# Optimization experiments

Hardware: AMD Instinct MI355X
Metric: run time of the kernel (lower is better)

## Reference

```python
import jax, jax.numpy as jnp
import numpy as np

B, T, F, H = 2048, 512, 32, 16  # batch, seq, input_size, hidden_size


def _gru_layer(x, W_ih, W_hh, b_ih, b_hh):
    # x: [B, T, in]; W_ih: [3H, in]; W_hh: [3H, H]
    xg = jnp.einsum('bti,gi->btg', x, W_ih) + b_ih  # [B, T, 3H] precomputed input gates

    def step(h, xg_t):
        hg = h @ W_hh.T + b_hh                      # [B, 3H]
        xr, xz, xn = jnp.split(xg_t, 3, axis=-1)
        hr, hz, hn = jnpp_split(hg) if False else jnp.split(hg, 3, axis=-1)
        r = jax.nn.sigmoid(xr + hr)
        z = jax.nn.sigmoid(xz + hz)
        n = jnp.tanh(xn + r * hn)
        h_new = (1.0 - z) * n + z * h
        return h_new, h_new

    h0 = jnp.zeros((x.shape[0], W_hh.shape[1]), x.dtype)
    _, hs = jax.lax.scan(step, h0, jnp.swapaxes(xg, 0, 1))  # [T, B, H]
    return jnp.swapaxes(hs, 0, 1)                            # [B, T, H]


def setup_inputs() -> dict:
    key = jax.random.key(0)
    ks = jax.random.split(key, 12)
    s = 1.0 / np.sqrt(H)
    u = lambda k, shape: jax.random.uniform(k, shape, jnp.float32, -s, s)
    return {
        'x': jax.random.normal(ks[0], (B, T, F), jnp.float32),
        'W_ih0': u(ks[1], (3 * H, F)),
        'W_hh0': u(ks[2], (3 * H, H)),
        'b_ih0': u(ks[3], (3 * H,)),
        'b_hh0': u(ks[4], (3 * H,)),
        'W_ih1': u(ks[5], (3 * H, H)),
        'W_hh1': u(ks[6], (3 * H, H)),
        'b_ih1': u(ks[7], (3 * H,)),
        'b_hh1': u(ks[8], (3 * H,)),
        'fc_w': u(ks[9], (1, H)),
        'fc_b': u(ks[10], (1,)),
    }


def reference(x, W_ih0, W_hh0, b_ih0, b_hh0, W_ih1, W_hh1, b_ih1, b_hh1, fc_w, fc_b):
    h1 = _gru_layer(x, W_ih0, W_hh0, b_ih0, b_hh0)   # [B, T, H]
    h2 = _gru_layer(h1, W_ih1, W_hh1, b_ih1, b_hh1)  # [B, T, H]
    return h2[:, -1, :] @ fc_w.T + fc_b              # [B, 1]
```

## Files before the change

### kernel.cpp

```cpp
#include <hip/hip_runtime.h>

static constexpr int T_LEN = 512;

typedef _Float16 h2 __attribute__((ext_vector_type(2)));

__device__ __forceinline__ float fsigm(float x) {
    return __builtin_amdgcn_rcpf(1.0f + __expf(-x));
}
__device__ __forceinline__ float ftanh(float x) {
    return 1.0f - 2.0f * __builtin_amdgcn_rcpf(1.0f + __expf(2.0f * x));
}
template <int CTRL>
__device__ __forceinline__ float rotf(float v) {
    return __builtin_bit_cast(float,
        __builtin_amdgcn_mov_dpp(__builtin_bit_cast(int, v), CTRL, 0xf, 0xf, true));
}
template <int CTRL>
__device__ __forceinline__ unsigned rotu(unsigned v) {
    return (unsigned)__builtin_amdgcn_mov_dpp((int)v, CTRL, 0xf, 0xf, true);
}
__device__ __forceinline__ unsigned pk2(float a, float b) {
    return __builtin_bit_cast(unsigned, __builtin_amdgcn_cvt_pkrtz(a, b));
}
__device__ __forceinline__ float dot2(float acc, unsigned w, unsigned p) {
    asm("v_dot2_f32_f16 %0, %1, %2, %0" : "+v"(acc) : "v"(w), "v"(p));
    return acc;
}

__global__ __launch_bounds__(256, 1) void gru2_dot(
    const float* __restrict__ x,
    const float* __restrict__ Wih0, const float* __restrict__ Whh0,
    const float* __restrict__ bih0, const float* __restrict__ bhh0,
    const float* __restrict__ Wih1, const float* __restrict__ Whh1,
    const float* __restrict__ bih1, const float* __restrict__ bhh1,
    const float* __restrict__ fcw,  const float* __restrict__ fcb,
    float* __restrict__ out)
{
    const int tid  = threadIdx.x;
    const int w    = tid >> 6;
    const int lane = tid & 63;
    const int j    = lane & 15;
    const int bb   = (w & 1) * 4 + (lane >> 4);
    const int b    = blockIdx.x * 8 + bb;
    const bool isL0 = (w < 2);

    __shared__ float h0buf[8][8][16];

    const int d1 = (((int)rotf<0x121>((float)j)) - j) & 15;

    unsigned WX[3][16];
    unsigned WH[3][8];
    unsigned WI[3][8];
    float B_r, B_z, B_in, B_hn;

    if (isL0) {
#pragma unroll
        for (int g = 0; g < 3; ++g) {
            const int row = g * 16 + j;
#pragma unroll
            for (int m = 0; m < 16; ++m) {
                const int c = (j + m * d1) & 15;
                WX[g][m] = pk2(Wih0[row * 32 + c], Wih0[row * 32 + 16 + c]);
            }
#pragma unroll
            for (int m = 0; m < 8; ++m) {
                const int c = (j + m * d1) & 15;
                const int c8 = (c + 8) & 15;
                WH[g][m] = pk2(Whh0[row * 16 + c], Whh0[row * 16 + c8]);
            }
        }
        B_r  = bih0[j]      + bhh0[j];
        B_z  = bih0[16 + j] + bhh0[16 + j];
        B_in = bih0[32 + j];
        B_hn = bhh0[32 + j];
    } else {
#pragma unroll
        for (int g = 0; g < 3; ++g) {
            const int row = g * 16 + j;
#pragma unroll
            for (int m = 0; m < 8; ++m) {
                const int c = (j + m * d1) & 15;
                const int c8 = (c + 8) & 15;
                WI[g][m] = pk2(Wih1[row * 16 + c], Wih1[row * 16 + c8]);
                WH[g][m] = pk2(Whh1[row * 16 + c], Whh1[row * 16 + c8]);
            }
        }
        B_r  = bih1[j]      + bhh1[j];
        B_z  = bih1[16 + j] + bhh1[16 + j];
        B_in = bih1[32 + j];
        B_hn = bhh1[32 + j];
    }

    float hs = 0.f;

    const float* xpf = x + (size_t)b * T_LEN * 32;
    float xa0, xh0, xa1, xh1, xa2, xh2, xa3, xh3;
    if (isL0) {
        xa0 = xpf[0 * 32 + j];  xh0 = xpf[0 * 32 + 16 + j];
        xa1 = xpf[1 * 32 + j];  xh1 = xpf[1 * 32 + 16 + j];
        xa2 = xpf[2 * 32 + j];  xh2 = xpf[2 * 32 + 16 + j];
        xa3 = xpf[3 * 32 + j];  xh3 = xpf[3 * 32 + 16 + j];
    }

    float* const lbase = &h0buf[0][bb][j];

    auto l0_step = [&](float& xa, float& xh, int k, float* lw) {
        unsigned p = pk2(xa, xh);
        xa = xpf[(4 + k) * 32 + j];
        xh = xpf[(4 + k) * 32 + 16 + j];

        float ar = B_r, az = B_z, an = B_in, hn = B_hn;
#pragma unroll
        for (int m = 0; m < 16; ++m) {
            ar = dot2(ar, WX[0][m], p);
            az = dot2(az, WX[1][m], p);
            an = dot2(an, WX[2][m], p);
            if (m < 15) p = rotu<0x121>(p);
        }
        unsigned q = pk2(hs, rotf<0x128>(hs));
#pragma unroll
        for (int m = 0; m < 8; ++m) {
            ar = dot2(ar, WH[0][m], q);
            az = dot2(az, WH[1][m], q);
            hn = dot2(hn, WH[2][m], q);
            if (m < 7) q = rotu<0x121>(q);
        }
        const float r = fsigm(ar);
        const float z = fsigm(az);
        const float n = ftanh(an + r * hn);
        hs = fmaf(z, hs - n, n);
        *lw = hs;
    };

    auto l1_step = [&](float u) {
        unsigned p0 = pk2(u, rotf<0x128>(u));
        unsigned p1 = pk2(hs, rotf<0x128>(hs));
        float ar = B_r, az = B_z, axn = B_in, ahn = B_hn;
#pragma unroll
        for (int m = 0; m < 8; ++m) {
            ar  = dot2(ar,  WI[0][m], p0);
            ar  = dot2(ar,  WH[0][m], p1);
            az  = dot2(az,  WI[1][m], p0);
            az  = dot2(az,  WH[1][m], p1);
            axn = dot2(axn, WI[2][m], p0);
            ahn = dot2(ahn, WH[2][m], p1);
            if (m < 7) { p0 = rotu<0x121>(p0); p1 = rotu<0x121>(p1); }
        }
        const float r = fsigm(ar);
        const float z = fsigm(az);
        const float n = ftanh(axn + r * ahn);
        hs = fmaf(z, hs - n, n);
    };

#pragma unroll 1
    for (int g = 0; g < 129; ++g) {
        if (isL0) {
            if (g < 128) {
                float* lw = lbase + ((g & 1) ? 4 : 0) * 128;
                l0_step(xa0, xh0, 0, lw + 0 * 128);
                l0_step(xa1, xh1, 1, lw + 1 * 128);
                l0_step(xa2, xh2, 2, lw + 2 * 128);
                l0_step(xa3, xh3, 3, lw + 3 * 128);
                xpf += (g < 126) ? 128 : 0;
            }
        } else {
            if (g > 0) {
                const float* lr = lbase + ((g & 1) ? 0 : 4) * 128;
                const float u0 = lr[0 * 128];
                const float u1 = lr[1 * 128];
                const float u2 = lr[2 * 128];
                const float u3 = lr[3 * 128];
                l1_step(u0);
                l1_step(u1);
                l1_step(u2);
                l1_step(u3);
            }
        }
        asm volatile("s_waitcnt lgkmcnt(0)\n\ts_barrier" ::: "memory");
    }

    if (!isL0) {
        float p = fcw[j] * hs;
        p += __shfl_xor(p, 1);
        p += __shfl_xor(p, 2);
        p += __shfl_xor(p, 4);
        p += __shfl_xor(p, 8);
        if (j == 0) out[b] = p + fcb[0];
    }
}

extern "C" void kernel_launch(void* const* d_in, const int* in_sizes, int n_in,
                              void* d_out, int out_size, void* d_ws, size_t ws_size,
                              hipStream_t stream) {
    const float* x    = (const float*)d_in[0];
    const float* Wih0 = (const float*)d_in[1];
    const float* Whh0 = (const float*)d_in[2];
    const float* bih0 = (const float*)d_in[3];
    const float* bhh0 = (const float*)d_in[4];
    const float* Wih1 = (const float*)d_in[5];
    const float* Whh1 = (const float*)d_in[6];
    const float* bih1 = (const float*)d_in[7];
    const float* bhh1 = (const float*)d_in[8];
    const float* fcw  = (const float*)d_in[9];
    const float* fcb  = (const float*)d_in[10];

    gru2_dot<<<256, 256, 0, stream>>>(x, Wih0, Whh0, bih0, bhh0,
                                      Wih1, Whh1, bih1, bhh1, fcw, fcb,
                                      (float*)d_out);
}
```

Measured before the change: 183.5 us.

## Balance layer0/layer1 waves by offloading input-gate projections to layer-1 waves

Layer-0 waves do much more work per step (a 16-wide input projection plus the recurrent part) than layer-1 waves. This change makes layer-1 waves precompute the layer-0 input-gate projections for two of every eight timesteps and pass them through shared memory. Layer 0 then runs a light step for those rows. Groups grow from four to eight steps per barrier, which halves the barrier count, at the cost of more shared memory and extra weight registers in layer-1 waves.

```diff
diff --git a/kernel.cpp b/kernel.cpp
--- a/kernel.cpp
+++ b/kernel.cpp
@@ -1,8 +1,6 @@
 #include <hip/hip_runtime.h>
 
 static constexpr int T_LEN = 512;
-
-typedef _Float16 h2 __attribute__((ext_vector_type(2)));
 
 __device__ __forceinline__ float fsigm(float x) {
     return __builtin_amdgcn_rcpf(1.0f + __expf(-x));
@@ -27,7 +25,7 @@
     return acc;
 }
 
-__global__ __launch_bounds__(256, 1) void gru2_dot(
+__global__ __launch_bounds__(256, 1) void gru2_bal(
     const float* __restrict__ x,
     const float* __restrict__ Wih0, const float* __restrict__ Whh0,
     const float* __restrict__ bih0, const float* __restrict__ bhh0,
@@ -44,16 +42,14 @@
     const int b    = blockIdx.x * 8 + bb;
     const bool isL0 = (w < 2);
 
-    __shared__ float h0buf[8][8][16];
+    __shared__ float h0buf[16][8][16];
+    __shared__ float xgbuf[2][2][3][8][16];
 
     const int d1 = (((int)rotf<0x121>((float)j)) - j) & 15;
-
-    unsigned WX[3][16];
-    unsigned WH[3][8];
-    unsigned WI[3][8];
-    float B_r, B_z, B_in, B_hn;
+    const float* xbase = x + (size_t)b * T_LEN * 32;
 
     if (isL0) {
+        unsigned WX[3][16], WH[3][8];
 #pragma unroll
         for (int g = 0; g < 3; ++g) {
             const int row = g * 16 + j;
@@ -65,15 +61,94 @@
 #pragma unroll
             for (int m = 0; m < 8; ++m) {
                 const int c = (j + m * d1) & 15;
-                const int c8 = (c + 8) & 15;
-                WH[g][m] = pk2(Whh0[row * 16 + c], Whh0[row * 16 + c8]);
-            }
-        }
-        B_r  = bih0[j]      + bhh0[j];
-        B_z  = bih0[16 + j] + bhh0[16 + j];
-        B_in = bih0[32 + j];
-        B_hn = bhh0[32 + j];
+                WH[g][m] = pk2(Whh0[row * 16 + c], Whh0[row * 16 + ((c + 8) & 15)]);
+            }
+        }
+        const float B_r  = bih0[j]      + bhh0[j];
+        const float B_z  = bih0[16 + j] + bhh0[16 + j];
+        const float B_in = bih0[32 + j];
+        const float B_hn = bhh0[32 + j];
+
+        float hs = 0.f;
+
+        float xa0 = xbase[0*32+j], xh0 = xbase[0*32+16+j];
+        float xa1 = xbase[1*32+j], xh1 = xbase[1*32+16+j];
+        float xa2 = xbase[2*32+j], xh2 = xbase[2*32+16+j];
+        float xa3 = xbase[3*32+j], xh3 = xbase[3*32+16+j];
+        float xa4 = xbase[4*32+j], xh4 = xbase[4*32+16+j];
+        float xa5 = xbase[5*32+j], xh5 = xbase[5*32+16+j];
+        float xa6 = xbase[6*32+j], xh6 = xbase[6*32+16+j];
+        float xa7 = xbase[7*32+j], xh7 = xbase[7*32+16+j];
+
+        auto heavy = [&](float& xa, float& xh, int row) {
+            unsigned p = pk2(xa, xh);
+            int pr = row + 8; if (pr > T_LEN - 1) pr = T_LEN - 1;
+            xa = xbase[pr * 32 + j];
+            xh = xbase[pr * 32 + 16 + j];
+            float ar = B_r, az = B_z, an = B_in, hn = B_hn;
+#pragma unroll
+            for (int m = 0; m < 16; ++m) {
+                ar = dot2(ar, WX[0][m], p);
+                az = dot2(az, WX[1][m], p);
+                an = dot2(an, WX[2][m], p);
+                if (m < 15) p = rotu<0x121>(p);
+            }
+            unsigned q = pk2(hs, rotf<0x128>(hs));
+#pragma unroll
+            for (int m = 0; m < 8; ++m) {
+                ar = dot2(ar, WH[0][m], q);
+                az = dot2(az, WH[1][m], q);
+                hn = dot2(hn, WH[2][m], q);
+                if (m < 7) q = rotu<0x121>(q);
+            }
+            const float r = fsigm(ar);
+            const float z = fsigm(az);
+            const float n = ftanh(an + r * hn);
+            hs = fmaf(z, hs - n, n);
+            h0buf[row & 15][bb][j] = hs;
+        };
+        auto light = [&](int row) {
+            const int par = (row >> 3) & 1, rb = row & 1;
+            float ar = xgbuf[par][rb][0][bb][j];
+            float az = xgbuf[par][rb][1][bb][j];
+            float an = xgbuf[par][rb][2][bb][j];
+            float hn = B_hn;
+            unsigned q = pk2(hs, rotf<0x128>(hs));
+#pragma unroll
+            for (int m = 0; m < 8; ++m) {
+                ar = dot2(ar, WH[0][m], q);
+                az = dot2(az, WH[1][m], q);
+                hn = dot2(hn, WH[2][m], q);
+                if (m < 7) q = rotu<0x121>(q);
+            }
+            const float r = fsigm(ar);
+            const float z = fsigm(az);
+            const float n = ftanh(an + r * hn);
+            hs = fmaf(z, hs - n, n);
+            h0buf[row & 15][bb][j] = hs;
+        };
+
+        heavy(xa0, xh0, 0); heavy(xa1, xh1, 1); heavy(xa2, xh2, 2);
+        heavy(xa3, xh3, 3); heavy(xa4, xh4, 4); heavy(xa5, xh5, 5);
+        heavy(xa6, xh6, 6); heavy(xa7, xh7, 7);
+        asm volatile("s_waitcnt lgkmcnt(0)\n\ts_barrier" ::: "memory");
+
+#pragma unroll 1
+        for (int G = 1; G < 64; ++G) {
+            const int r0 = 8 * G;
+            heavy(xa0, xh0, r0 + 0);
+            heavy(xa1, xh1, r0 + 1);
+            heavy(xa2, xh2, r0 + 2);
+            heavy(xa3, xh3, r0 + 3);
+            heavy(xa4, xh4, r0 + 4);
+            heavy(xa5, xh5, r0 + 5);
+            light(r0 + 6);
+            light(r0 + 7);
+            asm volatile("s_waitcnt lgkmcnt(0)\n\ts_barrier" ::: "memory");
+        }
+        asm volatile("s_waitcnt lgkmcnt(0)\n\ts_barrier" ::: "memory");
     } else {
+        unsigned WI[3][8], WHr[3][8], WX[3][16];
 #pragma unroll
         for (int g = 0; g < 3; ++g) {
             const int row = g * 16 + j;
@@ -81,105 +156,109 @@
             for (int m = 0; m < 8; ++m) {
                 const int c = (j + m * d1) & 15;
                 const int c8 = (c + 8) & 15;
-                WI[g][m] = pk2(Wih1[row * 16 + c], Wih1[row * 16 + c8]);
-                WH[g][m] = pk2(Whh1[row * 16 + c], Whh1[row * 16 + c8]);
-            }
-        }
-        B_r  = bih1[j]      + bhh1[j];
-        B_z  = bih1[16 + j] + bhh1[16 + j];
-        B_in = bih1[32 + j];
-        B_hn = bhh1[32 + j];
-    }
-
-    float hs = 0.f;
-
-    const float* xpf = x + (size_t)b * T_LEN * 32;
-    float xa0, xh0, xa1, xh1, xa2, xh2, xa3, xh3;
-    if (isL0) {
-        xa0 = xpf[0 * 32 + j];  xh0 = xpf[0 * 32 + 16 + j];
-        xa1 = xpf[1 * 32 + j];  xh1 = xpf[1 * 32 + 16 + j];
-        xa2 = xpf[2 * 32 + j];  xh2 = xpf[2 * 32 + 16 + j];
-        xa3 = xpf[3 * 32 + j];  xh3 = xpf[3 * 32 + 16 + j];
-    }
-
-    float* const lbase = &h0buf[0][bb][j];
-
-    auto l0_step = [&](float& xa, float& xh, int k, float* lw) {
-        unsigned p = pk2(xa, xh);
-        xa = xpf[(4 + k) * 32 + j];
-        xh = xpf[(4 + k) * 32 + 16 + j];
-
-        float ar = B_r, az = B_z, an = B_in, hn = B_hn;
-#pragma unroll
-        for (int m = 0; m < 16; ++m) {
-            ar = dot2(ar, WX[0][m], p);
-            az = dot2(az, WX[1][m], p);
-            an = dot2(an, WX[2][m], p);
-            if (m < 15) p = rotu<0x121>(p);
-        }
-        unsigned q = pk2(hs, rotf<0x128>(hs));
-#pragma unroll
-        for (int m = 0; m < 8; ++m) {
-            ar = dot2(ar, WH[0][m], q);
-            az = dot2(az, WH[1][m], q);
-            hn = dot2(hn, WH[2][m], q);
-            if (m < 7) q = rotu<0x121>(q);
-        }
-        const float r = fsigm(ar);
-        const float z = fsigm(az);
-        const float n = ftanh(an + r * hn);
-        hs = fmaf(z, hs - n, n);
-        *lw = hs;
-    };
-
-    auto l1_step = [&](float u) {
-        unsigned p0 = pk2(u, rotf<0x128>(u));
-        unsigned p1 = pk2(hs, rotf<0x128>(hs));
-        float ar = B_r, az = B_z, axn = B_in, ahn = B_hn;
-#pragma unroll
-        for (int m = 0; m < 8; ++m) {
-            ar  = dot2(ar,  WI[0][m], p0);
-            ar  = dot2(ar,  WH[0][m], p1);
-            az  = dot2(az,  WI[1][m], p0);
-            az  = dot2(az,  WH[1][m], p1);
-            axn = dot2(axn, WI[2][m], p0);
-            ahn = dot2(ahn, WH[2][m], p1);
-            if (m < 7) { p0 = rotu<0x121>(p0); p1 = rotu<0x121>(p1); }
-        }
-        const float r = fsigm(ar);
-        const float z = fsigm(az);
-        const float n = ftanh(axn + r * ahn);
-        hs = fmaf(z, hs - n, n);
-    };
+                WI[g][m]  = pk2(Wih1[row * 16 + c], Wih1[row * 16 + c8]);
+                WHr[g][m] = pk2(Whh1[row * 16 + c], Whh1[row * 16 + c8]);
+            }
+#pragma unroll
+            for (int m = 0; m < 16; ++m) {
+                const int c = (j + m * d1) & 15;
+                WX[g][m] = pk2(Wih0[row * 32 + c], Wih0[row * 32 + 16 + c]);
+            }
+        }
+        const float B_r  = bih1[j]      + bhh1[j];
+        const float B_z  = bih1[16 + j] + bhh1[16 + j];
+        const float B_in = bih1[32 + j];
+        const float B_hn = bhh1[32 + j];
+        const float BX_r = bih0[j]      + bhh0[j];
+        const float BX_z = bih0[16 + j] + bhh0[16 + j];
+        const float BX_n = bih0[32 + j];
+
+        float hs = 0.f;
+
+        float ya0 = xbase[14 * 32 + j], yh0 = xbase[14 * 32 + 16 + j];
+        float ya1 = xbase[15 * 32 + j], yh1 = xbase[15 * 32 + 16 + j];
+
+        auto l1_step = [&](float u) {
+            unsigned p0 = pk2(u,  rotf<0x128>(u));
+            unsigned p1 = pk2(hs, rotf<0x128>(hs));
+            float ar = B_r, az = B_z, axn = B_in, ahn = B_hn;
+#pragma unroll
+            for (int m = 0; m < 8; ++m) {
+                ar  = dot2(ar,  WI[0][m],  p0);
+                ar  = dot2(ar,  WHr[0][m], p1);
+                az  = dot2(az,  WI[1][m],  p0);
+                az  = dot2(az,  WHr[1][m], p1);
+                axn = dot2(axn, WI[2][m],  p0);
+                ahn = dot2(ahn, WHr[2][m], p1);
+                if (m < 7) { p0 = rotu<0x121>(p0); p1 = rotu<0x121>(p1); }
+            }
+            const float r = fsigm(ar);
+            const float z = fsigm(az);
+            const float n = ftanh(axn + r * ahn);
+            hs = fmaf(z, hs - n, n);
+        };
+        auto l1_xg = [&](float xa, float xh, int row) {
+            unsigned p = pk2(xa, xh);
+            float ar = BX_r, az = BX_z, an = BX_n;
+#pragma unroll
+            for (int m = 0; m < 16; ++m) {
+                ar = dot2(ar, WX[0][m], p);
+                az = dot2(az, WX[1][m], p);
+                an = dot2(an, WX[2][m], p);
+                if (m < 15) p = rotu<0x121>(p);
+            }
+            const int par = (row >> 3) & 1, rb = row & 1;
+            xgbuf[par][rb][0][bb][j] = ar;
+            xgbuf[par][rb][1][bb][j] = az;
+            xgbuf[par][rb][2][bb][j] = an;
+        };
+
+        l1_xg(ya0, yh0, 14);
+        l1_xg(ya1, yh1, 15);
+        ya0 = xbase[22 * 32 + j];  yh0 = xbase[22 * 32 + 16 + j];
+        ya1 = xbase[23 * 32 + j];  yh1 = xbase[23 * 32 + 16 + j];
+        asm volatile("s_waitcnt lgkmcnt(0)\n\ts_barrier" ::: "memory");
 
 #pragma unroll 1
-    for (int g = 0; g < 129; ++g) {
-        if (isL0) {
-            if (g < 128) {
-                float* lw = lbase + ((g & 1) ? 4 : 0) * 128;
-                l0_step(xa0, xh0, 0, lw + 0 * 128);
-                l0_step(xa1, xh1, 1, lw + 1 * 128);
-                l0_step(xa2, xh2, 2, lw + 2 * 128);
-                l0_step(xa3, xh3, 3, lw + 3 * 128);
-                xpf += (g < 126) ? 128 : 0;
-            }
-        } else {
-            if (g > 0) {
-                const float* lr = lbase + ((g & 1) ? 0 : 4) * 128;
-                const float u0 = lr[0 * 128];
-                const float u1 = lr[1 * 128];
-                const float u2 = lr[2 * 128];
-                const float u3 = lr[3 * 128];
-                l1_step(u0);
-                l1_step(u1);
-                l1_step(u2);
-                l1_step(u3);
-            }
-        }
-        asm volatile("s_waitcnt lgkmcnt(0)\n\ts_barrier" ::: "memory");
-    }
-
-    if (!isL0) {
+        for (int G = 1; G < 64; ++G) {
+            const int r0 = 8 * (G - 1);
+            const int s0 = r0 & 15;
+            const float u0 = h0buf[s0 + 0][bb][j];
+            const float u1 = h0buf[s0 + 1][bb][j];
+            const float u2 = h0buf[s0 + 2][bb][j];
+            const float u3 = h0buf[s0 + 3][bb][j];
+            const float u4 = h0buf[s0 + 4][bb][j];
+            const float u5 = h0buf[s0 + 5][bb][j];
+            const float u6 = h0buf[s0 + 6][bb][j];
+            const float u7 = h0buf[s0 + 7][bb][j];
+            l1_step(u0); l1_step(u1); l1_step(u2); l1_step(u3);
+            l1_step(u4); l1_step(u5); l1_step(u6); l1_step(u7);
+            if (G <= 62) {
+                const int rx = 8 * (G + 1) + 6;
+                l1_xg(ya0, yh0, rx);
+                l1_xg(ya1, yh1, rx + 1);
+                int pr = 8 * (G + 2) + 6;
+                if (pr > T_LEN - 2) pr = T_LEN - 2;
+                ya0 = xbase[pr * 32 + j];       yh0 = xbase[pr * 32 + 16 + j];
+                ya1 = xbase[(pr + 1) * 32 + j]; yh1 = xbase[(pr + 1) * 32 + 16 + j];
+            }
+            asm volatile("s_waitcnt lgkmcnt(0)\n\ts_barrier" ::: "memory");
+        }
+        {
+            const int s0 = 504 & 15;
+            const float u0 = h0buf[s0 + 0][bb][j];
+            const float u1 = h0buf[s0 + 1][bb][j];
+            const float u2 = h0buf[s0 + 2][bb][j];
+            const float u3 = h0buf[s0 + 3][bb][j];
+            const float u4 = h0buf[s0 + 4][bb][j];
+            const float u5 = h0buf[s0 + 5][bb][j];
+            const float u6 = h0buf[s0 + 6][bb][j];
+            const float u7 = h0buf[s0 + 7][bb][j];
+            l1_step(u0); l1_step(u1); l1_step(u2); l1_step(u3);
+            l1_step(u4); l1_step(u5); l1_step(u6); l1_step(u7);
+        }
+        asm volatile("s_waitcnt lgkmcnt(0)\n\ts_barrier" ::: "memory");
+
         float p = fcw[j] * hs;
         p += __shfl_xor(p, 1);
         p += __shfl_xor(p, 2);
@@ -204,7 +283,7 @@
     const float* fcw  = (const float*)d_in[9];
     const float* fcb  = (const float*)d_in[10];
 
-    gru2_dot<<<256, 256, 0, stream>>>(x, Wih0, Whh0, bih0, bhh0,
+    gru2_bal<<<256, 256, 0, stream>>>(x, Wih0, Whh0, bih0, bhh0,
                                       Wih1, Whh1, bih1, bhh1, fcw, fcb,
                                       (float*)d_out);
 }
```

Measured after the change: 150.9 us. 17.7% less time.
